# Optimization experiments

Hardware: AMD Instinct MI355X
Metric: run time of the kernel (lower is better)

## Reference

```python
import jax, jax.numpy as jnp
import numpy as np

HEAD_SIZE = 20
NUM_HEADS = 2


def setup_inputs() -> dict:
    key = jax.random.key(0)
    k1, k2, k3, k4, k5, k6 = jax.random.split(key, 6)
    N, L, D = 32, 256, HEAD_SIZE
    x = jax.random.normal(k1, (N, N, L, D), dtype=jnp.float32)
    y = jax.random.normal(k2, (N, N, L, D), dtype=jnp.float32)
    s = 1.0 / np.sqrt(D)
    WQ = jax.random.normal(k3, (D, HEAD_SIZE * NUM_HEADS), dtype=jnp.float32) * s
    WK = jax.random.normal(k4, (D, HEAD_SIZE * NUM_HEADS), dtype=jnp.float32) * s
    WV = jax.random.normal(k5, (D, HEAD_SIZE * NUM_HEADS), dtype=jnp.float32) * s
    WH = jax.random.normal(k6, (HEAD_SIZE * NUM_HEADS, HEAD_SIZE), dtype=jnp.float32) * s
    return {"x": x, "y": y, "WQ": WQ, "WK": WK, "WV": WV, "WH": WH}


def _masked_softmax(logits):
    # mask wherever the raw logit is exactly zero (custom zero-value mask)
    mask = logits != 0
    z = jnp.exp(logits - jnp.max(logits, axis=-1, keepdims=True))
    z = jnp.where(mask, z, jnp.zeros_like(z))
    return z / (jnp.sum(z, axis=-1, keepdims=True) + 1e-10)


def reference(x, y, WQ, WK, WV, WH):
    nSet_x, nSet_y, Lx, D = x.shape
    Ly = y.shape[2]
    H, Dh = NUM_HEADS, HEAD_SIZE
    scale = 1.0 / jnp.sqrt(jnp.asarray(Dh, dtype=jnp.float32))

    # cross branch: transpose x [1,0,2,3] then flatten set dims
    xq = jnp.transpose(x, (1, 0, 2, 3)).reshape(-1, Lx, D)  # [B, Lx, D]
    yf = y.reshape(-1, Ly, D)                               # [B, Ly, D]

    q = xq @ WQ   # [B, Lx, H*Dh]
    k = yf @ WK   # [B, Ly, H*Dh]
    v = yf @ WV   # [B, Ly, H*Dh]

    B = q.shape[0]
    q = q.reshape(B, Lx, H, Dh).transpose(0, 2, 1, 3)  # [B, H, Lx, Dh]
    k = k.reshape(B, Ly, H, Dh).transpose(0, 2, 1, 3)
    v = v.reshape(B, Ly, H, Dh).transpose(0, 2, 1, 3)

    logits = jnp.einsum('bhqd,bhkd->bhqk', q, k) * scale  # [B, H, Lx, Ly]
    attn = _masked_softmax(logits)
    o = jnp.einsum('bhqk,bhkd->bhqd', attn, v)            # [B, H, Lx, Dh]
    o = o.transpose(0, 2, 1, 3).reshape(B, Lx, H * Dh)
    out = o @ WH                                          # [B, Lx, Dh]

    out = out.reshape(nSet_x, nSet_y, Lx, Dh).transpose(1, 0, 2, 3)
    return out
```

## Files before the change

### kernel.cpp

```cpp
#include <hip/hip_runtime.h>
#include <stdint.h>


#define NSET 32
#define SEQL 256
#define DM   20
#define NH   2
#define DH   20

typedef __attribute__((ext_vector_type(8))) short short8;
typedef __attribute__((ext_vector_type(4))) short short4v;
typedef __attribute__((ext_vector_type(4))) float f32x4;

#define MFMA32(a, b, c) __builtin_amdgcn_mfma_f32_16x16x32_bf16((a), (b), (c), 0, 0, 0)

#if __has_builtin(__builtin_amdgcn_mfma_f32_16x16x16bf16_1k)
#define MFMA16(a, b, c) __builtin_amdgcn_mfma_f32_16x16x16bf16_1k((a), (b), (c), 0, 0, 0)
#elif __has_builtin(__builtin_amdgcn_mfma_f32_16x16x16_bf16)
#define MFMA16(a, b, c) __builtin_amdgcn_mfma_f32_16x16x16_bf16((a), (b), (c), 0, 0, 0)
#else
static __device__ __forceinline__ f32x4 MFMA16(short4v a, short4v b, f32x4 c) {
    asm volatile("s_nop 1\n\tv_mfma_f32_16x16x16_bf16 %0, %1, %2, %0\n\ts_nop 7"
                 : "+v"(c) : "v"(a), "v"(b));
    return c;
}
#endif

__device__ __forceinline__ uint32_t bfhu(float f) {
    return (__float_as_uint(f) + 0x8000u) >> 16;
}
__device__ __forceinline__ uint32_t packbf(float hi, float lo) {
    return __builtin_amdgcn_perm(__float_as_uint(hi) + 0x8000u,
                                 __float_as_uint(lo) + 0x8000u, 0x07060302u);
}
__device__ __forceinline__ float fexp2(float x) {
    float r;
    asm("v_exp_f32 %0, %1" : "=v"(r) : "v"(x));
    return r;
}

__device__ __forceinline__ short8 ldsA(const short* base, int row, int qd) {
    short8 f = {0, 0, 0, 0, 0, 0, 0, 0};
    if (qd < 3) f = *(const short8*)(base + row * 24 + qd * 8);
    return f;
}

__device__ __forceinline__ short8 gfrag(const float* rowp, int qd) {
    short8 f = {0, 0, 0, 0, 0, 0, 0, 0};
    if (qd < 2) {
        float4 a = *(const float4*)(rowp + qd * 8);
        float4 b = *(const float4*)(rowp + qd * 8 + 4);
        f[0] = (short)bfhu(a.x); f[1] = (short)bfhu(a.y);
        f[2] = (short)bfhu(a.z); f[3] = (short)bfhu(a.w);
        f[4] = (short)bfhu(b.x); f[5] = (short)bfhu(b.y);
        f[6] = (short)bfhu(b.z); f[7] = (short)bfhu(b.w);
    } else if (qd == 2) {
        float4 a = *(const float4*)(rowp + 16);
        f[0] = (short)bfhu(a.x); f[1] = (short)bfhu(a.y);
        f[2] = (short)bfhu(a.z); f[3] = (short)bfhu(a.w);
    }
    return f;
}

#define SMEM_BYTES 72320

__global__ __launch_bounds__(512, 4) void set_attn_v10(
    const float* __restrict__ x, const float* __restrict__ y,
    const float* __restrict__ wq, const float* __restrict__ wk,
    const float* __restrict__ wv, const float* __restrict__ wh,
    float* __restrict__ out)
{
    __shared__ __align__(16) char smem[SMEM_BYTES];
    short* sKb  = (short*)smem;
    short* sVtb = (short*)(smem + 24576);
    short* sWb  = (short*)(smem + 45696);
    float* sL   = (float*)(smem + 70272);
    float* sOut = (float*)smem;

    const int tid     = threadIdx.x;
    const int lane    = tid & 63;
    const int w       = tid >> 6;
    const int c       = lane & 15;
    const int qd      = lane >> 4;
    const int head    = w >> 2;
    const int rowbase = (w & 3) * 64;
    const int b       = blockIdx.x;
    const int bi      = b >> 5, bj = b & 31;

    short* myW = sWb + w * (64 * 24);
    short* sK  = sKb + head * (SEQL * 24);
    short* sVt = sVtb + head * (20 * 264);

    *(uint2*)(sKb + tid * 24 + 20) = make_uint2(0u, 0u);
    *(uint2*)(myW + lane * 24 + 20) = make_uint2(0u, 0u);

    const float QS = 0.22360679774997896f * 1.4426950408889634f;

    short8 xf[4];
#pragma unroll
    for (int mt = 0; mt < 4; ++mt)
        xf[mt] = gfrag(x + ((size_t)b * SEQL + rowbase + mt * 16 + c) * DM, qd);

    short8 wqf[2], wkf[2], wvf[2];
#pragma unroll
    for (int dt = 0; dt < 2; ++dt) {
        int n = dt * 16 + c;
        short8 fq = {0,0,0,0,0,0,0,0}, fk = fq, fv = fq;
        if (n < 20) {
#pragma unroll
            for (int j = 0; j < 8; ++j) {
                int k = qd * 8 + j;
                if (k < 20) {
                    fq[j] = (short)bfhu(wq[k * 40 + head * 20 + n]);
                    fk[j] = (short)bfhu(wk[k * 40 + head * 20 + n]);
                    fv[j] = (short)bfhu(wv[k * 40 + head * 20 + n]);
                }
            }
        }
        wqf[dt] = fq; wkf[dt] = fk; wvf[dt] = fv;
    }

#pragma unroll
    for (int mt = 0; mt < 4; ++mt) {
        int rb = rowbase + mt * 16;
        short8 yf = gfrag(y + ((size_t)(bj * NSET + bi) * SEQL + rb + c) * DM, qd);
#pragma unroll
        for (int dt = 0; dt < 2; ++dt) {
            f32x4 z = {0.f, 0.f, 0.f, 0.f};
            f32x4 kres = MFMA32(yf, wkf[dt], z);
            f32x4 vres = MFMA32(yf, wvf[dt], z);
            f32x4 qres = MFMA32(xf[mt], wqf[dt], z);
            int n = dt * 16 + c;
            if (n < 20) {
#pragma unroll
                for (int reg = 0; reg < 4; ++reg) {
                    sK[(rb + qd * 4 + reg) * 24 + n] = (short)bfhu(kres[reg]);
                    myW[(mt * 16 + qd * 4 + reg) * 24 + n] =
                        (short)bfhu(qres[reg] * QS);
                }
                uint2 pv = make_uint2(packbf(vres[1], vres[0]),
                                      packbf(vres[3], vres[2]));
                *(uint2*)(sVt + n * 264 + rb + qd * 4) = pv;
            }
        }
    }
    __syncthreads();

    short8 qb[4];
#pragma unroll
    for (int mt = 0; mt < 4; ++mt) qb[mt] = ldsA(myW, mt * 16 + c, qd);

    f32x4 oacc[4][2];
#pragma unroll
    for (int mt = 0; mt < 4; ++mt)
#pragma unroll
        for (int dt = 0; dt < 2; ++dt) oacc[mt][dt] = (f32x4){0.f, 0.f, 0.f, 0.f};
    float ls0 = 0.f, ls1 = 0.f, ls2 = 0.f, ls3 = 0.f;

    for (int s0 = 0; s0 < SEQL; s0 += 32) {
        short8 kf0 = ldsA(sK, s0 + c, qd);
        short8 kf1 = ldsA(sK, s0 + 16 + c, qd);
        short4v vb[2][2];
#pragma unroll
        for (int dt = 0; dt < 2; ++dt) {
            int d = dt * 16 + c;
#pragma unroll
            for (int st = 0; st < 2; ++st) {
                uint2 u = make_uint2(0u, 0u);
                if (d < 20)
                    u = *(const uint2*)(sVt + d * 264 + s0 + st * 16 + qd * 4);
                short4v t; *(uint2*)&t = u;
                vb[st][dt] = t;
            }
        }
#pragma unroll
        for (int mt = 0; mt < 4; ++mt) {
#pragma unroll
            for (int st = 0; st < 2; ++st) {
                f32x4 z = {0.f, 0.f, 0.f, 0.f};
                f32x4 sacc = MFMA32((st == 0 ? kf0 : kf1), qb[mt], z);
                float p0, p1, p2, p3;
                {
                    float v0 = sacc[0], v1 = sacc[1], v2 = sacc[2], v3 = sacc[3];
                    p0 = (v0 != 0.f) ? fexp2(v0) : 0.f;
                    p1 = (v1 != 0.f) ? fexp2(v1) : 0.f;
                    p2 = (v2 != 0.f) ? fexp2(v2) : 0.f;
                    p3 = (v3 != 0.f) ? fexp2(v3) : 0.f;
                }
                float lsum = (p0 + p1) + (p2 + p3);
                if (mt == 0) ls0 += lsum;
                else if (mt == 1) ls1 += lsum;
                else if (mt == 2) ls2 += lsum;
                else ls3 += lsum;
                short4v pf;
                *(uint2*)&pf = make_uint2(packbf(p1, p0), packbf(p3, p2));
                oacc[mt][0] = MFMA16(pf, vb[st][0], oacc[mt][0]);
                oacc[mt][1] = MFMA16(pf, vb[st][1], oacc[mt][1]);
            }
        }
    }

    ls0 += __shfl_xor(ls0, 16, 64); ls0 += __shfl_xor(ls0, 32, 64);
    ls1 += __shfl_xor(ls1, 16, 64); ls1 += __shfl_xor(ls1, 32, 64);
    ls2 += __shfl_xor(ls2, 16, 64); ls2 += __shfl_xor(ls2, 32, 64);
    ls3 += __shfl_xor(ls3, 16, 64); ls3 += __shfl_xor(ls3, 32, 64);
    float sel = ls0;
    if (qd == 1) sel = ls1;
    if (qd == 2) sel = ls2;
    if (qd == 3) sel = ls3;
    sL[w * 64 + lane] = sel;
    __syncthreads();

    short8 whf[2];
#pragma unroll
    for (int dt = 0; dt < 2; ++dt) {
        int n = dt * 16 + c;
        short8 f = {0,0,0,0,0,0,0,0};
        if (n < 20) {
#pragma unroll
            for (int j = 0; j < 8; ++j) {
                int k = qd * 8 + j;
                if (k < 20) f[j] = (short)bfhu(wh[(head * 20 + k) * 20 + n]);
            }
        }
        whf[dt] = f;
    }
#pragma unroll
    for (int mt = 0; mt < 4; ++mt) {
        float inv[4];
#pragma unroll
        for (int reg = 0; reg < 4; ++reg)
            inv[reg] = 1.f / (sL[w * 64 + mt * 16 + qd * 4 + reg] + 1e-10f);
#pragma unroll
        for (int dt = 0; dt < 2; ++dt) {
            int n = dt * 16 + c;
            if (n < 20) {
#pragma unroll
                for (int reg = 0; reg < 4; ++reg)
                    myW[(mt * 16 + qd * 4 + reg) * 24 + n] =
                        (short)bfhu(oacc[mt][dt][reg] * inv[reg]);
            }
        }
    }
    __syncthreads();

    f32x4 outacc[4][2];
#pragma unroll
    for (int mt = 0; mt < 4; ++mt) {
        short8 of = ldsA(myW, mt * 16 + c, qd);
        f32x4 z = {0.f, 0.f, 0.f, 0.f};
        outacc[mt][0] = MFMA32(of, whf[0], z);
        outacc[mt][1] = MFMA32(of, whf[1], z);
    }
    __syncthreads();

    if (head == 1) {
#pragma unroll
        for (int mt = 0; mt < 4; ++mt)
#pragma unroll
            for (int dt = 0; dt < 2; ++dt) {
                int n = dt * 16 + c;
                if (n < 20) {
#pragma unroll
                    for (int reg = 0; reg < 4; ++reg) {
                        int row = rowbase + mt * 16 + qd * 4 + reg;
                        sOut[row * 20 + n] = outacc[mt][dt][reg];
                    }
                }
            }
    }
    __syncthreads();

    if (head == 0) {
        float* ob = out + (size_t)b * (SEQL * DH);
#pragma unroll
        for (int mt = 0; mt < 4; ++mt)
#pragma unroll
            for (int dt = 0; dt < 2; ++dt) {
                int n = dt * 16 + c;
                if (n < 20) {
#pragma unroll
                    for (int reg = 0; reg < 4; ++reg) {
                        int row = rowbase + mt * 16 + qd * 4 + reg;
                        ob[row * 20 + n] = outacc[mt][dt][reg] + sOut[row * 20 + n];
                    }
                }
            }
    }
}

extern "C" void kernel_launch(void* const* d_in, const int* in_sizes, int n_in,
                              void* d_out, int out_size, void* d_ws, size_t ws_size,
                              hipStream_t stream) {
    const float* x  = (const float*)d_in[0];
    const float* y  = (const float*)d_in[1];
    const float* wq = (const float*)d_in[2];
    const float* wk = (const float*)d_in[3];
    const float* wv = (const float*)d_in[4];
    const float* wh = (const float*)d_in[5];
    float* out = (float*)d_out;

    set_attn_v10<<<dim3(NSET * NSET), dim3(512), 0, stream>>>(x, y, wq, wk, wv, wh, out);
}
```

Measured before the change: 142.8 us.

## Build Q fragments in registers via transposed MFMA and cross-lane permutes

Q is now computed as a transposed MFMA (W^T x X^T), and the result is rearranged into A-operand fragments with ds_bpermute, so it no longer round-trips through a per-wave shared-memory staging buffer. The O staging buffer is aliased onto the K region, which is dead by then. Together these shrink LDS from about 72KB to about 48KB per block, which may allow more resident blocks per CU and removes LDS stores and loads for Q. The cost is extra permute instructions, select logic and some register pressure.

Measured after the change: 147.3 us. +3.2%, slower.

```diff
diff --git a/kernel.cpp b/kernel.cpp
--- a/kernel.cpp
+++ b/kernel.cpp
@@ -62,9 +62,9 @@
     return f;
 }
 
-#define SMEM_BYTES 72320
-
-__global__ __launch_bounds__(512, 4) void set_attn_v10(
+#define SMEM_BYTES 47744
+
+__global__ __launch_bounds__(512, 4) void set_attn_v11(
     const float* __restrict__ x, const float* __restrict__ y,
     const float* __restrict__ wq, const float* __restrict__ wk,
     const float* __restrict__ wv, const float* __restrict__ wh,
@@ -73,8 +73,7 @@
     __shared__ __align__(16) char smem[SMEM_BYTES];
     short* sKb  = (short*)smem;
     short* sVtb = (short*)(smem + 24576);
-    short* sWb  = (short*)(smem + 45696);
-    float* sL   = (float*)(smem + 70272);
+    float* sL   = (float*)(smem + 45696);
     float* sOut = (float*)smem;
 
     const int tid     = threadIdx.x;
@@ -87,12 +86,11 @@
     const int b       = blockIdx.x;
     const int bi      = b >> 5, bj = b & 31;
 
-    short* myW = sWb + w * (64 * 24);
     short* sK  = sKb + head * (SEQL * 24);
     short* sVt = sVtb + head * (20 * 264);
+    short* myO = sKb + w * (64 * 24);
 
     *(uint2*)(sKb + tid * 24 + 20) = make_uint2(0u, 0u);
-    *(uint2*)(myW + lane * 24 + 20) = make_uint2(0u, 0u);
 
     const float QS = 0.22360679774997896f * 1.4426950408889634f;
 
@@ -101,25 +99,39 @@
     for (int mt = 0; mt < 4; ++mt)
         xf[mt] = gfrag(x + ((size_t)b * SEQL + rowbase + mt * 16 + c) * DM, qd);
 
-    short8 wqf[2], wkf[2], wvf[2];
+    short8 wqA0 = {0,0,0,0,0,0,0,0}, wqA1 = wqA0;
+#pragma unroll
+    for (int j = 0; j < 8; ++j) {
+        int k = qd * 8 + j;
+        if (k < 20) {
+            wqA0[j] = (short)bfhu(wq[k * 40 + head * 20 + c]);
+            if (c < 4) wqA1[j] = (short)bfhu(wq[k * 40 + head * 20 + 16 + c]);
+        }
+    }
+
+    short8 wkf[2], wvf[2];
 #pragma unroll
     for (int dt = 0; dt < 2; ++dt) {
         int n = dt * 16 + c;
-        short8 fq = {0,0,0,0,0,0,0,0}, fk = fq, fv = fq;
+        short8 fk = {0,0,0,0,0,0,0,0}, fv = fk;
         if (n < 20) {
 #pragma unroll
             for (int j = 0; j < 8; ++j) {
                 int k = qd * 8 + j;
                 if (k < 20) {
-                    fq[j] = (short)bfhu(wq[k * 40 + head * 20 + n]);
                     fk[j] = (short)bfhu(wk[k * 40 + head * 20 + n]);
                     fv[j] = (short)bfhu(wv[k * 40 + head * 20 + n]);
                 }
             }
         }
-        wqf[dt] = fq; wkf[dt] = fk; wvf[dt] = fv;
-    }
-
+        wkf[dt] = fk; wvf[dt] = fv;
+    }
+
+    const int i01 = (c + ((qd & 1) << 5)) << 2;
+    const int i23 = (c + 16 + ((qd & 1) << 5)) << 2;
+    const int iB  = c << 2;
+
+    short8 qb[4];
 #pragma unroll
     for (int mt = 0; mt < 4; ++mt) {
         int rb = rowbase + mt * 16;
@@ -129,26 +141,41 @@
             f32x4 z = {0.f, 0.f, 0.f, 0.f};
             f32x4 kres = MFMA32(yf, wkf[dt], z);
             f32x4 vres = MFMA32(yf, wvf[dt], z);
-            f32x4 qres = MFMA32(xf[mt], wqf[dt], z);
             int n = dt * 16 + c;
             if (n < 20) {
 #pragma unroll
-                for (int reg = 0; reg < 4; ++reg) {
+                for (int reg = 0; reg < 4; ++reg)
                     sK[(rb + qd * 4 + reg) * 24 + n] = (short)bfhu(kres[reg]);
-                    myW[(mt * 16 + qd * 4 + reg) * 24 + n] =
-                        (short)bfhu(qres[reg] * QS);
-                }
                 uint2 pv = make_uint2(packbf(vres[1], vres[0]),
                                       packbf(vres[3], vres[2]));
                 *(uint2*)(sVt + n * 264 + rb + qd * 4) = pv;
             }
         }
-    }
-    __syncthreads();
-
-    short8 qb[4];
-#pragma unroll
-    for (int mt = 0; mt < 4; ++mt) qb[mt] = ldsA(myW, mt * 16 + c, qd);
+        {
+            f32x4 z = {0.f, 0.f, 0.f, 0.f};
+            f32x4 ra = MFMA32(wqA0, xf[mt], z);
+            f32x4 rb2 = MFMA32(wqA1, xf[mt], z);
+            uint32_t dwA0 = packbf(ra[1] * QS, ra[0] * QS);
+            uint32_t dwA1 = packbf(ra[3] * QS, ra[2] * QS);
+            uint32_t dwB0 = packbf(rb2[1] * QS, rb2[0] * QS);
+            uint32_t dwB1 = packbf(rb2[3] * QS, rb2[2] * QS);
+            uint32_t t0a = (uint32_t)__builtin_amdgcn_ds_bpermute(i01, (int)dwA0);
+            uint32_t t1a = (uint32_t)__builtin_amdgcn_ds_bpermute(i01, (int)dwA1);
+            uint32_t t0b = (uint32_t)__builtin_amdgcn_ds_bpermute(iB, (int)dwB0);
+            uint32_t t1b = (uint32_t)__builtin_amdgcn_ds_bpermute(iB, (int)dwB1);
+            uint32_t t2  = (uint32_t)__builtin_amdgcn_ds_bpermute(i23, (int)dwA0);
+            uint32_t t3  = (uint32_t)__builtin_amdgcn_ds_bpermute(i23, (int)dwA1);
+            uint32_t q0 = qd < 2 ? t0a : (qd == 2 ? t0b : 0u);
+            uint32_t q1 = qd < 2 ? t1a : (qd == 2 ? t1b : 0u);
+            uint32_t q2 = qd < 2 ? t2 : 0u;
+            uint32_t q3 = qd < 2 ? t3 : 0u;
+            short8 f;
+            *(uint2*)&f = make_uint2(q0, q1);
+            *(((uint2*)&f) + 1) = make_uint2(q2, q3);
+            qb[mt] = f;
+        }
+    }
+    __syncthreads();
 
     f32x4 oacc[4][2];
 #pragma unroll
@@ -237,7 +264,7 @@
             if (n < 20) {
 #pragma unroll
                 for (int reg = 0; reg < 4; ++reg)
-                    myW[(mt * 16 + qd * 4 + reg) * 24 + n] =
+                    myO[(mt * 16 + qd * 4 + reg) * 24 + n] =
                         (short)bfhu(oacc[mt][dt][reg] * inv[reg]);
             }
         }
@@ -247,7 +274,7 @@
     f32x4 outacc[4][2];
 #pragma unroll
     for (int mt = 0; mt < 4; ++mt) {
-        short8 of = ldsA(myW, mt * 16 + c, qd);
+        short8 of = ldsA(myO, mt * 16 + c, qd);
         f32x4 z = {0.f, 0.f, 0.f, 0.f};
         outacc[mt][0] = MFMA32(of, whf[0], z);
         outacc[mt][1] = MFMA32(of, whf[1], z);
@@ -300,5 +327,5 @@
     const float* wh = (const float*)d_in[5];
     float* out = (float*)d_out;
 
-    set_attn_v10<<<dim3(NSET * NSET), dim3(512), 0, stream>>>(x, y, wq, wk, wv, wh, out);
-}
+    set_attn_v11<<<dim3(NSET * NSET), dim3(512), 0, stream>>>(x, y, wq, wk, wv, wh, out);
+}
```
